# Kernel tuning notes

Measured on AMD Instinct MI355X. Metric: run time of the kernel, lower is better.

The kernel has to match this reference:

```python
import jax, jax.numpy as jnp
import numpy as np

B, L, F, H, HDE, E, V, MH, MW, TOUT = 64, 2, 512, 512, 512, 512, 94, 6, 40, 30
V2 = V + 2          # vocab + START/END + NULL slots
T = TOUT + 2        # decode steps
HW = MH * MW
START = V + 1
END = V + 1


def setup_inputs() -> dict:
    key = jax.random.key(0)
    ks = jax.random.split(key, 20)
    s = 0.05  # weight scale for numerical stability
    n = lambda k, shape: jax.random.normal(k, shape, jnp.float32) * s
    d = {}
    d['conv_f'] = jax.random.normal(ks[0], (B, F, MH, MW), jnp.float32)
    d['target'] = jax.random.randint(ks[1], (B, TOUT), 0, 95, dtype=jnp.int32)
    d['w_ih_en'] = n(ks[2], (L, 4 * H, F))
    d['w_hh_en'] = n(ks[3], (L, 4 * H, H))
    d['b_ih_en'] = n(ks[4], (L, 4 * H))
    d['b_hh_en'] = n(ks[5], (L, 4 * H))
    d['embed_w'] = n(ks[6], (V2, H))
    d['w_ih_de'] = n(ks[7], (L, 4 * HDE, H))
    d['w_hh_de'] = n(ks[8], (L, 4 * HDE, HDE))
    d['b_ih_de'] = n(ks[9], (L, 4 * HDE))
    d['b_hh_de'] = n(ks[10], (L, 4 * HDE))
    d['att_wh'] = n(ks[11], (E, HDE))
    d['att_bh'] = n(ks[12], (E,))
    d['att_conv_w'] = n(ks[13], (E, F, 3, 3))
    d['att_conv_b'] = n(ks[14], (E,))
    d['att_wv'] = n(ks[15], (1, E))
    d['att_bv'] = n(ks[16], (1,))
    d['out_w'] = n(ks[17], (V2, HDE + F))
    d['out_b'] = n(ks[18], (V2,))
    return d


def _lstm_cell(x, h, c, wih, whh, bih, bhh):
    # PyTorch gate order: i, f, g, o
    g = x @ wih.T + h @ whh.T + bih + bhh
    i, f, gg, o = jnp.split(g, 4, axis=-1)
    c_new = jax.nn.sigmoid(f) * c + jax.nn.sigmoid(i) * jnp.tanh(gg)
    h_new = jax.nn.sigmoid(o) * jnp.tanh(c_new)
    return h_new, c_new


def _forward(conv_f, target, w_ih_en, w_hh_en, b_ih_en, b_hh_en, embed_w,
             w_ih_de, w_hh_de, b_ih_de, b_hh_de, att_wh, att_bh,
             att_conv_w, att_conv_b, att_wv, att_bv, out_w, out_b):
    # ---- encoder: maxpool over full height, then 2-layer LSTM over width ----
    x_seq = jnp.max(conv_f, axis=2).transpose(2, 0, 1)  # [W, B, F]

    def enc_step(carry, xt):
        h, c = carry
        inp = xt
        hs, cs = [], []
        for l in range(L):
            hl, cl = _lstm_cell(inp, h[l], c[l], w_ih_en[l], w_hh_en[l],
                                b_ih_en[l], b_hh_en[l])
            inp = hl
            hs.append(hl); cs.append(cl)
        return (jnp.stack(hs), jnp.stack(cs)), inp

    z = jnp.zeros((L, B, H), conv_f.dtype)
    _, enc_out = jax.lax.scan(enc_step, (z, z), x_seq)
    holistic = enc_out[-1]  # [B, H]

    # ---- attention: conv_f embedding computed ONCE (invariant across steps) ----
    xe = jax.lax.conv_general_dilated(
        conv_f, att_conv_w, (1, 1), 'SAME',
        dimension_numbers=('NCHW', 'OIHW', 'NCHW')) + att_conv_b[None, :, None, None]
    x_em = xe.reshape(B, E, HW).transpose(0, 2, 1)       # [B, HW, E]
    cf_flat = conv_f.reshape(B, F, HW).transpose(0, 2, 1)  # [B, HW, F]

    # ---- decoder inputs: t=0 holistic, t>=1 embed(gt_with_start[:, t-1]) ----
    gt = jnp.concatenate(
        [jnp.full((B, 1), START, dtype=target.dtype), target], axis=1)  # [B, T-1]
    xs = jnp.concatenate([holistic[None], embed_w[gt.T]], axis=0)  # [T, B, H]

    def dec_step(carry, xt):
        h, c = carry
        inp = xt
        hs, cs = [], []
        for l in range(L):
            hl, cl = _lstm_cell(inp, h[l], c[l], w_ih_de[l], w_hh_de[l],
                                b_ih_de[l], b_hh_de[l])
            inp = hl
            hs.append(hl); cs.append(cl)
        hlast = inp  # [B, HDE]
        g_em = hlast @ att_wh.T + att_bh                    # [B, E]
        feat = jnp.tanh(x_em + g_em[:, None, :])            # [B, HW, E] (dropout=identity)
        e = feat @ att_wv[0] + att_bv[0]                    # [B, HW]
        alpha = jax.nn.softmax(e, axis=-1)
        att = jnp.einsum('bw,bwf->bf', alpha, cf_flat)      # [B, F]
        logits = jnp.concatenate([hlast, att], axis=-1) @ out_w.T + out_b
        scores = jax.nn.log_softmax(logits, axis=-1)        # [B, V2]
        return (jnp.stack(hs), jnp.stack(cs)), scores

    zd = jnp.zeros((B, HDE), conv_f.dtype)
    z0 = jnp.stack([zd] * L)
    _, out_tbv = jax.lax.scan(dec_step, (z0, z0), xs)  # [T, B, V2]
    out = out_tbv.transpose(1, 0, 2)                    # [B, T, V2]

    # ---- build l_target: [0, target..., 0] with first padding 0 -> END ----
    l_target = jnp.zeros((B, T), jnp.int32).at[:, 1:-1].set(target)
    j = jnp.argmax(l_target[:, 1:] == 0, axis=1) + 1  # first zero at col>=1 (always exists)
    l_target = l_target.at[jnp.arange(B), j].set(END)

    # ---- masked NLL loss ----
    lt = l_target.reshape(-1)
    nll = -out.reshape(-1, V2)[jnp.arange(B * T), lt]
    mask = (lt != 0).astype(out.dtype)
    return jnp.sum(nll * mask) / jnp.sum(mask)


def reference(conv_f, target, w_ih_en, w_hh_en, b_ih_en, b_hh_en, embed_w,
              w_ih_de, w_hh_de, b_ih_de, b_hh_de, att_wh, att_bh,
              att_conv_w, att_conv_b, att_wv, att_bv, out_w, out_b):
    return _forward(conv_f, target, w_ih_en, w_hh_en, b_ih_en, b_hh_en, embed_w,
                    w_ih_de, w_hh_de, b_ih_de, b_hh_de, att_wh, att_bh,
                    att_conv_w, att_conv_b, att_wv, att_bv, out_w, out_b)
```

## Files before the change

### kernel.cpp

```cpp
#include <hip/hip_runtime.h>

typedef __fp16 f16;
typedef __fp16 f16x4 __attribute__((ext_vector_type(4)));
typedef __fp16 f16x8 __attribute__((ext_vector_type(8)));
typedef float  f32x4 __attribute__((ext_vector_type(4)));
typedef unsigned long long ull;

#define DEV static __device__ __forceinline__

DEV f32x4 mfma16(f16x4 a, f16x4 b, f32x4 c) {
  return __builtin_amdgcn_mfma_f32_16x16x16f16(a, b, c, 0, 0, 0);
}
DEV f16x4 lo4(f16x8 v) { return __builtin_shufflevector(v, v, 0, 1, 2, 3); }
DEV f16x4 hi4(f16x8 v) { return __builtin_shufflevector(v, v, 4, 5, 6, 7); }
DEV float sigf(float x) { return 1.f / (1.f + __expf(-x)); }
DEV float tanh_(float x) { float e = __expf(2.f * x); return 1.f - 2.f / (e + 1.f); }

union U8 { float4 f4; float2 f2[2]; };
union H2 { unsigned u; f16 h[2]; };
union H4 { ull u; f16 h[4]; f16x4 v; };

#define HB 32768

DEV ull ldU(const ull* p) {
  return __hip_atomic_load(p, __ATOMIC_RELAXED, __HIP_MEMORY_SCOPE_AGENT);
}
DEV unsigned ldF(const unsigned* p) {
  return __hip_atomic_load(p, __ATOMIC_RELAXED, __HIP_MEMORY_SCOPE_AGENT);
}
DEV void stU32(unsigned* p, unsigned v) {
  __hip_atomic_store(p, v, __ATOMIC_RELAXED, __HIP_MEMORY_SCOPE_AGENT);
}
DEV void stU64(ull* p, ull v) {
  __hip_atomic_store(p, v, __ATOMIC_RELAXED, __HIP_MEMORY_SCOPE_AGENT);
}

DEV void wait8(const unsigned* line, unsigned tgt) {
  if (threadIdx.x < 8)
    while (ldF(line + threadIdx.x * 16) < tgt) {}
  __syncthreads();
}

DEV void signalDone(unsigned* line, int slot) {
  asm volatile("s_waitcnt vmcnt(0)" ::: "memory");
  __syncthreads();
  if (threadIdx.x == 0)
    __hip_atomic_fetch_add(line + slot * 16, 1u, __ATOMIC_RELAXED, __HIP_MEMORY_SCOPE_AGENT);
}

DEV void stageRow(const f16* __restrict__ s, f16* __restrict__ dstRow, int ch) {
  U8 u0, u1;
  u0.f4 = *(const float4*)s;
  u1.f4 = *(const float4*)(s + 8);
  *(float2*)(dstRow +  0 + ch * 4) = u0.f2[0];
  *(float2*)(dstRow + 16 + ch * 4) = u0.f2[1];
  *(float2*)(dstRow + 32 + ch * 4) = u1.f2[0];
  *(float2*)(dstRow + 48 + ch * 4) = u1.f2[1];
}

DEV void stageAu(const ull* __restrict__ srcU, f16 (*A)[64][72], int tid) {
  int row = tid >> 2, ch = tid & 3;
  const ull* s = srcU + row * 128 + ch * 4;
#pragma unroll
  for (int c = 0; c < 8; ++c) {
    ull d0 = ldU(s + c * 16 + 0);
    ull d1 = ldU(s + c * 16 + 1);
    ull d2 = ldU(s + c * 16 + 2);
    ull d3 = ldU(s + c * 16 + 3);
    f16* d = &A[c][row][0];
    *(ull*)(d +  0 + ch * 4) = d0;
    *(ull*)(d + 16 + ch * 4) = d1;
    *(ull*)(d + 32 + ch * 4) = d2;
    *(ull*)(d + 48 + ch * 4) = d3;
  }
}

DEV void kloop32(const f16 (*Wt)[32][72], const f16 (*A)[64][72],
                 int mh, int ns, int m16, int g4, f32x4 acc[2]) {
#pragma unroll
  for (int c = 0; c < 8; ++c) {
#pragma unroll
    for (int half = 0; half < 2; ++half) {
      f16x8 bf = *(const f16x8*)&Wt[c][ns * 16 + m16][g4 * 16 + half * 8];
      f16x4 bl = lo4(bf), bh = hi4(bf);
#pragma unroll
      for (int mt = 0; mt < 2; ++mt) {
        f16x8 af = *(const f16x8*)&A[c][mh * 32 + mt * 16 + m16][g4 * 16 + half * 8];
        acc[mt] = mfma16(lo4(af), bl, acc[mt]);
        acc[mt] = mfma16(hi4(af), bh, acc[mt]);
      }
    }
  }
}

DEV void kloop64(const f16* Wg, const f16 (*A)[64][72],
                 int nsG, int m16, int g4, f32x4 acc[4]) {
#pragma unroll
  for (int c = 0; c < 8; ++c) {
#pragma unroll
    for (int half = 0; half < 2; ++half) {
      f16x8 bf = *(const f16x8*)&Wg[((size_t)(c * 64 + nsG * 16 + m16)) * 72 + g4 * 16 + half * 8];
      f16x4 bl = lo4(bf), bh = hi4(bf);
#pragma unroll
      for (int mt = 0; mt < 4; ++mt) {
        f16x8 af = *(const f16x8*)&A[c][mt * 16 + m16][g4 * 16 + half * 8];
        acc[mt] = mfma16(lo4(af), bl, acc[mt]);
        acc[mt] = mfma16(hi4(af), bh, acc[mt]);
      }
    }
  }
}

DEV void convTile(char* smem, int tile, const f16* __restrict__ cfT,
                  const f16* __restrict__ wc9, const float* __restrict__ cb,
                  f16* __restrict__ xemH) {
  f16 (*At)[40] = (f16(*)[40])smem;
  f16 (*Bt)[40] = (f16(*)[40])(smem + 19200);
  const int t = threadIdx.x, lane = t & 63, w = t >> 6;
  const int b = tile >> 2, eb = (tile & 3) * 128;
  const int m16 = lane & 15, g4 = lane >> 4;
  f32x4 acc[15][2] = {};

  for (int kr = 0; kr < 9; ++kr) {
    int dh = kr / 3 - 1, dw = kr % 3 - 1;
    for (int f0 = 0; f0 < 512; f0 += 32) {
      __syncthreads();
      if (t < 240) {
        int hh = t / 40 + dh, ww = t % 40 + dw;
        if (hh >= 0 && hh < 6 && ww >= 0 && ww < 40) {
          const f16* s = cfT + ((size_t)(b * 240 + hh * 40 + ww) * 512 + f0);
          U8 u0, u1, u2, u3;
          u0.f4 = *(const float4*)s;        u1.f4 = *(const float4*)(s + 8);
          u2.f4 = *(const float4*)(s + 16); u3.f4 = *(const float4*)(s + 24);
          *(float2*)&At[t][ 0] = u0.f2[0];
          *(float2*)&At[t][ 8] = u0.f2[1];
          *(float2*)&At[t][16] = u1.f2[0];
          *(float2*)&At[t][24] = u1.f2[1];
          *(float2*)&At[t][ 4] = u2.f2[0];
          *(float2*)&At[t][12] = u2.f2[1];
          *(float2*)&At[t][20] = u3.f2[0];
          *(float2*)&At[t][28] = u3.f2[1];
        } else {
          float2 z = make_float2(0.f, 0.f);
          *(float2*)&At[t][ 0] = z; *(float2*)&At[t][ 8] = z;
          *(float2*)&At[t][16] = z; *(float2*)&At[t][24] = z;
          *(float2*)&At[t][ 4] = z; *(float2*)&At[t][12] = z;
          *(float2*)&At[t][20] = z; *(float2*)&At[t][28] = z;
        }
      }
      {
        int n = t >> 1, ch = t & 1;
        const f16* s = wc9 + (size_t)(eb + n) * 4608 + kr * 512 + f0 + ch * 16;
        U8 u0, u1;
        u0.f4 = *(const float4*)s; u1.f4 = *(const float4*)(s + 8);
        *(float2*)&Bt[n][ 0 + ch * 4] = u0.f2[0];
        *(float2*)&Bt[n][ 8 + ch * 4] = u0.f2[1];
        *(float2*)&Bt[n][16 + ch * 4] = u1.f2[0];
        *(float2*)&Bt[n][24 + ch * 4] = u1.f2[1];
      }
      __syncthreads();
      f16x8 b0 = *(const f16x8*)&Bt[w * 32 + m16][g4 * 8];
      f16x8 b1v = *(const f16x8*)&Bt[w * 32 + 16 + m16][g4 * 8];
      f16x4 b0l = lo4(b0), b0h = hi4(b0), b1l = lo4(b1v), b1h = hi4(b1v);
#pragma unroll
      for (int mt = 0; mt < 15; ++mt) {
        f16x8 af = *(const f16x8*)&At[mt * 16 + m16][g4 * 8];
        f16x4 al = lo4(af), ah = hi4(af);
        acc[mt][0] = mfma16(al, b0l, acc[mt][0]);
        acc[mt][1] = mfma16(al, b1l, acc[mt][1]);
        acc[mt][0] = mfma16(ah, b0h, acc[mt][0]);
        acc[mt][1] = mfma16(ah, b1h, acc[mt][1]);
      }
    }
  }
#pragma unroll
  for (int nt = 0; nt < 2; ++nt) {
    int e = eb + w * 32 + nt * 16 + m16;
    float bias = cb[e];
#pragma unroll
    for (int mt = 0; mt < 15; ++mt)
#pragma unroll
      for (int r = 0; r < 4; ++r) {
        int p = mt * 16 + g4 * 4 + r;
        xemH[((size_t)(b * 240 + p)) * 512 + e] = (f16)(acc[mt][nt][r] + bias);
      }
  }
}


__global__ void k_convert4(const float* __restrict__ src, f16* __restrict__ dst, int n4) {
  int i = blockIdx.x * 256 + threadIdx.x;
  if (i < n4) {
    float4 v = ((const float4*)src)[i];
    f16x4 o = { (f16)v.x, (f16)v.y, (f16)v.z, (f16)v.w };
    *(f16x4*)(dst + (size_t)i * 4) = o;
  }
}

__global__ void k_convW(const float* __restrict__ s0, const float* __restrict__ s1,
                        const float* __restrict__ s2, const float* __restrict__ s3,
                        f16* __restrict__ d0, f16* __restrict__ d1,
                        f16* __restrict__ d2, f16* __restrict__ d3) {
  int i = blockIdx.x * 256 + threadIdx.x;
  int sel = i >> 19, j = i & 524287;
  const float* s = sel == 0 ? s0 : sel == 1 ? s1 : sel == 2 ? s2 : s3;
  f16* d = sel == 0 ? d0 : sel == 1 ? d1 : sel == 2 ? d2 : d3;
  float4 v = ((const float4*)s)[j];
  f16x4 o = { (f16)v.x, (f16)v.y, (f16)v.z, (f16)v.w };
  *(f16x4*)(d + (size_t)j * 4) = o;
}

__global__ void k_wc9(const float* __restrict__ src, f16* __restrict__ dst) {
  int i = blockIdx.x * 256 + threadIdx.x;
  if (i < 512 * 4608) {
    int e = i / 4608, k = i % 4608;
    int rr = k / 512, f = k % 512;
    dst[i] = (f16)src[(size_t)e * 4608 + f * 9 + rr];
  }
}

__global__ __launch_bounds__(256) void k_cfmx(
    const float* __restrict__ cf, f16* __restrict__ cfT, f16* __restrict__ xseq)
{
  __shared__ float sT[64][244];
  const int tid = threadIdx.x;
  const int f0 = blockIdx.x * 64, b = blockIdx.y;
  const float* src = cf + ((size_t)b * 512 + f0) * 240;
  for (int i = tid; i < 3840; i += 256) {
    float4 v = ((const float4*)src)[i];
    int fl = i / 60, pc = (i % 60) * 4;
    sT[fl][pc] = v.x; sT[fl][pc + 1] = v.y; sT[fl][pc + 2] = v.z; sT[fl][pc + 3] = v.w;
  }
  __syncthreads();
  if (tid < 240) {
    int p = tid;
    f16* drow = cfT + ((size_t)b * 240 + p) * 512 + f0;
#pragma unroll
    for (int j = 0; j < 8; ++j) {
      f16x8 o;
#pragma unroll
      for (int k = 0; k < 8; ++k) o[k] = (f16)sT[j * 8 + k][p];
      *(f16x8*)(drow + j * 8) = o;
    }
  }
  {
    int fl = tid >> 2, wq = tid & 3;
#pragma unroll
    for (int wi = 0; wi < 10; ++wi) {
      int w = wq * 10 + wi;
      float m = sT[fl][w];
#pragma unroll
      for (int h = 1; h < 6; ++h) m = fmaxf(m, sT[fl][h * 40 + w]);
      xseq[((size_t)w * 64 + b) * 512 + f0 + fl] = (f16)m;
    }
  }
}

__global__ void k_ltarget(const int* __restrict__ target, int* __restrict__ lt) {
  int b = threadIdx.x;
  if (b >= 64) return;
  int row[32];
  row[0] = 0;
  for (int t = 1; t <= 30; ++t) row[t] = target[b * 30 + t - 1];
  row[31] = 0;
  int j = 1;
  while (row[j] != 0) ++j;
  row[j] = 95;
  for (int t = 0; t < 32; ++t) lt[b * 32 + t] = row[t];
}

__global__ void k_fill_xs(const f16* __restrict__ hol, const f16* __restrict__ emb,
                          const int* __restrict__ tgt, f16* __restrict__ xs) {
  int i = blockIdx.x * 256 + threadIdx.x;
  if (i < 32 * 64 * 512) {
    int t = i / (64 * 512), r = i % (64 * 512);
    int b = r / 512, u = r % 512;
    f16 v;
    if (t == 0) v = hol[b * 512 + u];
    else {
      int tok = (t == 1) ? 95 : tgt[b * 30 + t - 2];
      v = emb[(size_t)tok * 512 + u];
    }
    xs[i] = v;
  }
}

__global__ __launch_bounds__(256) void k_gemmX(
    const f16* __restrict__ A, const f16* __restrict__ W,
    const float* __restrict__ b1, const float* __restrict__ b2,
    f16* __restrict__ C)
{
  __shared__ f16 At[64][72];
  __shared__ f16 Bt[64][72];
  const int t = threadIdx.x, lane = t & 63, g = t >> 6;
  f32x4 acc[4] = {};
  const int m16 = lane & 15, g4 = lane >> 4;
  const size_t arow0 = (size_t)blockIdx.x * 64;

  for (int k0 = 0; k0 < 512; k0 += 64) {
    __syncthreads();
    { int row = t >> 2, ch = t & 3;
      stageRow(A + (arow0 + row) * 512 + k0 + ch * 16, &At[row][0], ch); }
    { int row = t >> 2, ch = t & 3;
      stageRow(W + ((size_t)blockIdx.y * 64 + row) * 512 + k0 + ch * 16, &Bt[row][0], ch); }
    __syncthreads();
#pragma unroll
    for (int half = 0; half < 2; ++half) {
      f16x8 bf = *(const f16x8*)&Bt[g * 16 + m16][g4 * 16 + half * 8];
      f16x4 bl = lo4(bf), bh = hi4(bf);
#pragma unroll
      for (int mt = 0; mt < 4; ++mt) {
        f16x8 af = *(const f16x8*)&At[mt * 16 + m16][g4 * 16 + half * 8];
        acc[mt] = mfma16(lo4(af), bl, acc[mt]);
        acc[mt] = mfma16(hi4(af), bh, acc[mt]);
      }
    }
  }
  int e = blockIdx.y * 64 + g * 16 + m16;
  float bias = b1[e] + b2[e];
#pragma unroll
  for (int mt = 0; mt < 4; ++mt)
#pragma unroll
    for (int r = 0; r < 4; ++r)
      C[(arow0 + mt * 16 + g4 * 4 + r) * 2048 + e] = (f16)(acc[mt][r] + bias);
}

__global__ __launch_bounds__(256) void k_gemmG(
    const f16* __restrict__ A, const f16* __restrict__ W,
    const float* __restrict__ b1, f16* __restrict__ C)
{
  __shared__ f16 At[64][72];
  __shared__ f16 Bt[64][72];
  const int t = threadIdx.x, lane = t & 63, g = t >> 6;
  f32x4 acc[4] = {};
  const int m16 = lane & 15, g4 = lane >> 4;
  const size_t arow0 = (size_t)blockIdx.x * 64;

  for (int k0 = 0; k0 < 512; k0 += 64) {
    __syncthreads();
    { int row = t >> 2, ch = t & 3;
      stageRow(A + (arow0 + row) * 512 + k0 + ch * 16, &At[row][0], ch); }
    { int row = t >> 2, ch = t & 3;
      stageRow(W + ((size_t)blockIdx.y * 64 + row) * 512 + k0 + ch * 16, &Bt[row][0], ch); }
    __syncthreads();
#pragma unroll
    for (int half = 0; half < 2; ++half) {
      f16x8 bf = *(const f16x8*)&Bt[g * 16 + m16][g4 * 16 + half * 8];
      f16x4 bl = lo4(bf), bh = hi4(bf);
#pragma unroll
      for (int mt = 0; mt < 4; ++mt) {
        f16x8 af = *(const f16x8*)&At[mt * 16 + m16][g4 * 16 + half * 8];
        acc[mt] = mfma16(lo4(af), bl, acc[mt]);
        acc[mt] = mfma16(hi4(af), bh, acc[mt]);
      }
    }
  }
  int e = blockIdx.y * 64 + g * 16 + m16;
  float bias = b1[e];
#pragma unroll
  for (int mt = 0; mt < 4; ++mt)
#pragma unroll
    for (int r = 0; r < 4; ++r)
      C[(arow0 + mt * 16 + g4 * 4 + r) * 512 + e] = (f16)(acc[mt][r] + bias);
}

__global__ __launch_bounds__(256) void k_gemmL(
    const f16* __restrict__ A, const f16* __restrict__ W,
    const float* __restrict__ bias, float* __restrict__ C)
{
  __shared__ f16 At[64][72];
  __shared__ f16 Bt[64][72];
  const int t = threadIdx.x, lane = t & 63, g = t >> 6;
  f32x4 acc[4] = {};
  const int m16 = lane & 15, g4 = lane >> 4;
  const size_t arow0 = (size_t)blockIdx.x * 64;

  for (int k0 = 0; k0 < 1024; k0 += 64) {
    __syncthreads();
    { int row = t >> 2, ch = t & 3;
      stageRow(A + (arow0 + row) * 1024 + k0 + ch * 16, &At[row][0], ch); }
    { int row = t >> 2, ch = t & 3;
      stageRow(W + ((size_t)(blockIdx.y * 64 + row)) * 1024 + k0 + ch * 16, &Bt[row][0], ch); }
    __syncthreads();
#pragma unroll
    for (int half = 0; half < 2; ++half) {
      f16x8 bf = *(const f16x8*)&Bt[g * 16 + m16][g4 * 16 + half * 8];
      f16x4 bl = lo4(bf), bh = hi4(bf);
#pragma unroll
      for (int mt = 0; mt < 4; ++mt) {
        f16x8 af = *(const f16x8*)&At[mt * 16 + m16][g4 * 16 + half * 8];
        acc[mt] = mfma16(lo4(af), bl, acc[mt]);
        acc[mt] = mfma16(hi4(af), bh, acc[mt]);
      }
    }
  }
  int e = blockIdx.y * 64 + g * 16 + m16;
  if (e < 96) {
    float be = bias[e];
#pragma unroll
    for (int mt = 0; mt < 4; ++mt)
#pragma unroll
      for (int r = 0; r < 4; ++r)
        C[(arow0 + mt * 16 + g4 * 4 + r) * 96 + e] = acc[mt][r] + be;
  }
}

__global__ __launch_bounds__(256, 1) void k_lstm(
    int T,
    const f16* __restrict__ G0, const f16* __restrict__ whh0,
    const f16* __restrict__ wih1, const f16* __restrict__ whh1,
    const float* __restrict__ bih1, const float* __restrict__ bhh1,
    f16* __restrict__ h0seq, f16* __restrict__ h1seq,
    unsigned* __restrict__ cnt,
    const f16* __restrict__ cfT, const f16* __restrict__ wc9,
    const float* __restrict__ cb, f16* __restrict__ xemH, int convBase)
{
  __shared__ __align__(16) char smem[147456];
  const int tid = threadIdx.x, lane = tid & 63, w = tid >> 6;
  const int m16 = lane & 15, g4 = lane >> 4;
  const int bid = blockIdx.x;

  if (bid >= 96) {
    convTile(smem, convBase + bid - 96, cfT, wc9, cb, xemH);
    return;
  }

  if (bid < 32) {
    f16 (*sW)[64][72] = (f16(*)[64][72])smem;
    f16 (*sA)[64][72] = (f16(*)[64][72])(smem + 73728);
    float* sG = (float*)(smem + 73728);
    const int utile = bid;
    { int r = tid >> 2, ch = tid & 3;
      int grow = (r >> 4) * 512 + utile * 16 + (r & 15);
      for (int c = 0; c < 8; ++c)
        stageRow(whh0 + (size_t)grow * 512 + c * 64 + ch * 16, &sW[c][r][0], ch);
    }
    const int pb = tid >> 2, uq = tid & 3;
    float cst[4] = {0.f, 0.f, 0.f, 0.f};
    for (int t = 0; t < T; ++t) {
      if (t > 0) wait8(cnt + (t - 1) * 128, 4);
      stageAu((const ull*)h0seq + (size_t)t * 8192, sA, tid);
      __syncthreads();
      f32x4 acc[4] = {};
      kloop64((const f16*)sW, sA, w, m16, g4, acc);
      __syncthreads();
#pragma unroll
      for (int mt = 0; mt < 4; ++mt)
#pragma unroll
        for (int r = 0; r < 4; ++r)
          sG[((size_t)w * 64 + mt * 16 + g4 * 4 + r) * 17 + m16] = acc[mt][r];
      __syncthreads();
      {
        const f16* gp = G0 + ((size_t)(t * 64 + pb)) * 2048 + utile * 16 + uq * 4;
        H4 gI, gF, gG, gO, outp;
        gI.v = *(const f16x4*)(gp);
        gF.v = *(const f16x4*)(gp + 512);
        gG.v = *(const f16x4*)(gp + 1024);
        gO.v = *(const f16x4*)(gp + 1536);
#pragma unroll
        for (int j = 0; j < 4; ++j) {
          int u = uq * 4 + j;
          float gi = sG[(0 * 64 + pb) * 17 + u] + (float)gI.h[j];
          float gf = sG[(1 * 64 + pb) * 17 + u] + (float)gF.h[j];
          float gg = sG[(2 * 64 + pb) * 17 + u] + (float)gG.h[j];
          float go = sG[(3 * 64 + pb) * 17 + u] + (float)gO.h[j];
          float cn = sigf(gf) * cst[j] + sigf(gi) * tanh_(gg);
          float hn = sigf(go) * tanh_(cn);
          cst[j] = cn;
          outp.h[j] = (f16)hn;
        }
        stU64((ull*)h0seq + (size_t)(t + 1) * 8192 + pb * 128 + utile * 4 + uq, outp.u);
      }
      signalDone(cnt + t * 128, bid & 7);
    }
  } else {
    f16 (*sW2)[8][32][72] = (f16(*)[8][32][72])smem;
    f16 (*sA)[64][72] = (f16(*)[64][72])(smem + 73728);
    float* sG = (float*)(smem + 73728);
    const int utile = bid - 32;
    const int mh = w >> 1, ns = w & 1;
    { int mat = tid >> 7;
      int r = (tid >> 2) & 31, ch = tid & 3;
      int grow = (r >> 3) * 512 + utile * 8 + (r & 7);
      const f16* Wsrc = (mat == 0) ? wih1 : whh1;
      for (int c = 0; c < 8; ++c)
        stageRow(Wsrc + (size_t)grow * 512 + c * 64 + ch * 16, &sW2[mat][c][r][0], ch);
    }
    const int pb = tid >> 2, pup = tid & 3;
    float badd[4][2];
#pragma unroll
    for (int g = 0; g < 4; ++g)
#pragma unroll
      for (int j = 0; j < 2; ++j) {
        int rr = g * 512 + utile * 8 + pup * 2 + j;
        badd[g][j] = bih1[rr] + bhh1[rr];
      }
    float cst[2] = {0.f, 0.f};
    unsigned* line1 = cnt + (size_t)T * 128;
    for (int t = 0; t < T; ++t) {
      wait8(cnt + t * 128, 4);
      stageAu((const ull*)h0seq + (size_t)(t + 1) * 8192, sA, tid);
      if (t > 0) wait8(line1 + (t - 1) * 128, 8);
      else       __syncthreads();
      ull rg[8][4];
      { const ull* s1p = (const ull*)h1seq + (size_t)t * 8192 + (tid >> 2) * 128 + (tid & 3) * 4;
#pragma unroll
        for (int c = 0; c < 8; ++c)
#pragma unroll
          for (int q = 0; q < 4; ++q) rg[c][q] = ldU(s1p + c * 16 + q);
      }
      f32x4 acc[2] = {};
      kloop32(sW2[0], sA, mh, ns, m16, g4, acc);
      __syncthreads();
      { int row = tid >> 2, ch = tid & 3;
#pragma unroll
        for (int c = 0; c < 8; ++c) {
          f16* d = &sA[c][row][0];
          *(ull*)(d +  0 + ch * 4) = rg[c][0];
          *(ull*)(d + 16 + ch * 4) = rg[c][1];
          *(ull*)(d + 32 + ch * 4) = rg[c][2];
          *(ull*)(d + 48 + ch * 4) = rg[c][3];
        }
      }
      __syncthreads();
      kloop32(sW2[1], sA, mh, ns, m16, g4, acc);
      __syncthreads();
      { int nl = ns * 16 + m16;
#pragma unroll
        for (int mt = 0; mt < 2; ++mt)
#pragma unroll
          for (int r = 0; r < 4; ++r) {
            int b = mh * 32 + mt * 16 + g4 * 4 + r;
            sG[((nl >> 3) * 64 + b) * 9 + (nl & 7)] = acc[mt][r];
          }
      }
      __syncthreads();
      {
        H2 outp;
#pragma unroll
        for (int j = 0; j < 2; ++j) {
          int u = pup * 2 + j;
          float gi = sG[(0 * 64 + pb) * 9 + u] + badd[0][j];
          float gf = sG[(1 * 64 + pb) * 9 + u] + badd[1][j];
          float gg = sG[(2 * 64 + pb) * 9 + u] + badd[2][j];
          float go = sG[(3 * 64 + pb) * 9 + u] + badd[3][j];
          float cn = sigf(gf) * cst[j] + sigf(gi) * tanh_(gg);
          float hn = sigf(go) * tanh_(cn);
          cst[j] = cn;
          outp.h[j] = (f16)hn;
        }
        stU32((unsigned*)h1seq + (size_t)(t + 1) * 16384 + pb * 256 + utile * 4 + pup, outp.u);
      }
      signalDone(line1 + t * 128, bid & 7);
    }
  }
}


__global__ __launch_bounds__(256) void k_scoreAll(
    const f16* __restrict__ xemH, const f16* __restrict__ gAll,
    const float* __restrict__ wv, float* __restrict__ esc)
{
  __shared__ f16 sX[20][512];
  const int tid = threadIdx.x, lane = tid & 63, w = tid >> 6;
  const int tile = blockIdx.x, b = blockIdx.y;
  for (int i = tid; i < 20 * 64; i += 256) {
    int row = i >> 6, seg = i & 63;
    *(f16x8*)&sX[row][seg * 8] =
        *(const f16x8*)(xemH + ((size_t)(b * 240 + tile * 20 + row)) * 512 + seg * 8);
  }
  float w8[8];
  { const float4* wp = (const float4*)(wv + lane * 8);
    float4 wa = wp[0], wb = wp[1];
    w8[0] = wa.x; w8[1] = wa.y; w8[2] = wa.z; w8[3] = wa.w;
    w8[4] = wb.x; w8[5] = wb.y; w8[6] = wb.z; w8[7] = wb.w; }
  __syncthreads();
  for (int t = 0; t < 32; ++t) {
    f16x8 gv = *(const f16x8*)(gAll + ((size_t)(t * 64 + b)) * 512 + lane * 8);
    float g8[8];
#pragma unroll
    for (int j = 0; j < 8; ++j) g8[j] = (float)gv[j];
#pragma unroll
    for (int i = 0; i < 5; ++i) {
      int rr = i * 4 + w;
      f16x8 xv = *(const f16x8*)&sX[rr][lane * 8];
      float s = 0.f;
#pragma unroll
      for (int j = 0; j < 8; ++j) s += tanh_((float)xv[j] + g8[j]) * w8[j];
#pragma unroll
      for (int m = 32; m; m >>= 1) s += __shfl_xor(s, m);
      if (lane == 0) esc[((size_t)(t * 64 + b)) * 240 + tile * 20 + rr] = s;
    }
  }
}

__global__ __launch_bounds__(256) void k_smctx(
    const float* __restrict__ esc, const f16* __restrict__ cfT,
    const f16* __restrict__ h1seq, f16* __restrict__ ctx)
{
  __shared__ float aAl[8][240];
  const int tid = threadIdx.x, lane = tid & 63, w = tid >> 6;
  const int tq = blockIdx.x, b = blockIdx.y;
  for (int half = 0; half < 2; ++half) {
    int tt = w + half * 4;
    int t = tq * 8 + tt;
    const float* er = esc + ((size_t)(t * 64 + b)) * 240;
    float v[4];
    float mx = -1e30f;
#pragma unroll
    for (int q = 0; q < 4; ++q) {
      int p = lane + q * 64;
      v[q] = (p < 240) ? er[p] : -1e30f;
      mx = fmaxf(mx, v[q]);
    }
#pragma unroll
    for (int m = 32; m; m >>= 1) mx = fmaxf(mx, __shfl_xor(mx, m));
    float sum = 0.f;
#pragma unroll
    for (int q = 0; q < 4; ++q) { v[q] = __expf(v[q] - mx); sum += v[q]; }
#pragma unroll
    for (int m = 32; m; m >>= 1) sum += __shfl_xor(sum, m);
    float inv = 1.f / sum;
#pragma unroll
    for (int q = 0; q < 4; ++q) {
      int p = lane + q * 64;
      if (p < 240) aAl[tt][p] = v[q] * inv;
    }
  }
  __syncthreads();
  float acc[8][2] = {};
  const f16* cb = cfT + (size_t)b * 240 * 512;
  for (int p = 0; p < 240; ++p) {
    H2 cw; cw.u = *(const unsigned*)(cb + (size_t)p * 512 + tid * 2);
    float c0 = (float)cw.h[0], c1 = (float)cw.h[1];
#pragma unroll
    for (int tt = 0; tt < 8; ++tt) {
      float a = aAl[tt][p];
      acc[tt][0] += a * c0;
      acc[tt][1] += a * c1;
    }
  }
#pragma unroll
  for (int tt = 0; tt < 8; ++tt) {
    int t = tq * 8 + tt;
    size_t r = (size_t)(t * 64 + b);
    H2 o; o.h[0] = (f16)acc[tt][0]; o.h[1] = (f16)acc[tt][1];
    *(unsigned*)(ctx + r * 1024 + 512 + tid * 2) = o.u;
    *(unsigned*)(ctx + r * 1024 + tid * 2) =
        *(const unsigned*)(h1seq + (size_t)(t + 1) * HB + b * 512 + tid * 2);
  }
}

__global__ void k_nllloss(const float* __restrict__ lgt, const int* __restrict__ ltg,
                          float* __restrict__ out) {
  __shared__ float sa[256], sb[256];
  int tid = threadIdx.x;
  float a = 0.f, m = 0.f;
  for (int r = tid; r < 2048; r += 256) {
    int t = r >> 6, b = r & 63;
    int tok = ltg[b * 32 + t];
    if (tok != 0) {
      const float* row = lgt + (size_t)r * 96;
      float mx = -1e30f;
      for (int j = 0; j < 96; ++j) mx = fmaxf(mx, row[j]);
      float s = 0.f;
      for (int j = 0; j < 96; ++j) s += __expf(row[j] - mx);
      a += mx + __logf(s) - row[tok];
      m += 1.f;
    }
  }
  sa[tid] = a; sb[tid] = m; __syncthreads();
  for (int s = 128; s; s >>= 1) { if (tid < s) { sa[tid] += sa[tid + s]; sb[tid] += sb[tid + s]; } __syncthreads(); }
  if (tid == 0) out[0] = sa[0] / sb[0];
}


extern "C" void kernel_launch(void* const* d_in, const int* in_sizes, int n_in,
                              void* d_out, int out_size, void* d_ws, size_t ws_size,
                              hipStream_t stream) {
  (void)in_sizes; (void)n_in; (void)out_size; (void)ws_size;
  const float* conv_f = (const float*)d_in[0];
  const int*   target = (const int*)d_in[1];
  const float* wih_en = (const float*)d_in[2];
  const float* whh_en = (const float*)d_in[3];
  const float* bih_en = (const float*)d_in[4];
  const float* bhh_en = (const float*)d_in[5];
  const float* embed  = (const float*)d_in[6];
  const float* wih_de = (const float*)d_in[7];
  const float* whh_de = (const float*)d_in[8];
  const float* bih_de = (const float*)d_in[9];
  const float* bhh_de = (const float*)d_in[10];
  const float* att_wh = (const float*)d_in[11];
  const float* att_bh = (const float*)d_in[12];
  const float* att_cw = (const float*)d_in[13];
  const float* att_cb = (const float*)d_in[14];
  const float* att_wv = (const float*)d_in[15];
  const float* out_w  = (const float*)d_in[17];
  const float* out_b  = (const float*)d_in[18];
  float* out = (float*)d_out;

  size_t o = 0;
  char* base = (char*)d_ws;
  auto take = [&](size_t bytes) -> void* {
    void* p = base + o;
    o += (bytes + 255) & ~(size_t)255;
    return p;
  };
  const size_t WSZ = (size_t)2048 * 512;
  f16* wihEn = (f16*)take(2 * WSZ * 2);
  f16* whhEn = (f16*)take(2 * WSZ * 2);
  f16* wihDe = (f16*)take(2 * WSZ * 2);
  f16* whhDe = (f16*)take(2 * WSZ * 2);
  f16* awh   = (f16*)take((size_t)512 * 512 * 2);
  f16* emb   = (f16*)take((size_t)96 * 512 * 2);
  f16* wc9   = (f16*)take((size_t)512 * 4608 * 2);
  f16* cfT   = (f16*)take((size_t)64 * 240 * 512 * 2);
  f16* xseq  = (f16*)take((size_t)40 * 64 * 512 * 2);
  f16* xs    = (f16*)take((size_t)32 * 64 * 512 * 2);
  f16* xemH  = (f16*)take((size_t)64 * 240 * 512 * 2);
  f16* outwH = (f16*)take((size_t)128 * 1024 * 2);
  f16* X0en  = (f16*)take((size_t)2560 * 2048 * 2);
  f16* X0de  = (f16*)take((size_t)2048 * 2048 * 2);
  f16* h0seqE = (f16*)take((size_t)41 * HB * 2);
  f16* h1seqE = (f16*)take((size_t)41 * HB * 2);
  f16* h0seqD = (f16*)take((size_t)33 * HB * 2);
  f16* h1seqD = (f16*)take((size_t)33 * HB * 2);
  f16* gAll   = (f16*)take((size_t)2048 * 512 * 2);
  int*   ltg   = (int*)take((size_t)2048 * 4);
  unsigned* cntE = (unsigned*)take(65536);
  unsigned* cntD = (unsigned*)take(65536);
  float* escAll = (float*)X0en;
  float* lgtAll = (float*)((char*)X0en + 4194304);
  f16*   ctxAll = X0de;

  k_convW<<<8192, 256, 0, stream>>>(wih_en, whh_en, wih_de, whh_de,
                                    wihEn, whhEn, wihDe, whhDe);
  k_convert4<<<256, 256, 0, stream>>>(att_wh, awh, 512 * 512 / 4);
  k_convert4<<<48, 256, 0, stream>>>(embed, emb, 96 * 512 / 4);
  k_convert4<<<96, 256, 0, stream>>>(out_w, outwH, 96 * 1024 / 4);
  k_wc9<<<(512 * 4608 + 255) / 256, 256, 0, stream>>>(att_cw, wc9);
  k_cfmx<<<dim3(8, 64), 256, 0, stream>>>(conv_f, cfT, xseq);
  k_ltarget<<<1, 64, 0, stream>>>(target, ltg);
  hipMemsetAsync(h0seqE, 0, (size_t)HB * 2, stream);
  hipMemsetAsync(h1seqE, 0, (size_t)HB * 2, stream);
  hipMemsetAsync(h0seqD, 0, (size_t)HB * 2, stream);
  hipMemsetAsync(h1seqD, 0, (size_t)HB * 2, stream);
  hipMemsetAsync(cntE, 0, 131072, stream);

  k_gemmX<<<dim3(40, 32), 256, 0, stream>>>(xseq, wihEn, bih_en, bhh_en, X0en);

  k_lstm<<<224, 256, 0, stream>>>(40, X0en, whhEn, wihEn + WSZ, whhEn + WSZ,
                                  bih_en + 2048, bhh_en + 2048, h0seqE, h1seqE, cntE,
                                  cfT, wc9, att_cb, xemH, 0);

  k_fill_xs<<<(32 * 64 * 512 + 255) / 256, 256, 0, stream>>>(h1seqE + (size_t)40 * HB, emb, target, xs);
  k_gemmX<<<dim3(32, 32), 256, 0, stream>>>(xs, wihDe, bih_de, bhh_de, X0de);

  k_lstm<<<224, 256, 0, stream>>>(32, X0de, whhDe, wihDe + WSZ, whhDe + WSZ,
                                  bih_de + 2048, bhh_de + 2048, h0seqD, h1seqD, cntD,
                                  cfT, wc9, att_cb, xemH, 128);

  k_gemmG<<<dim3(32, 8), 256, 0, stream>>>(h1seqD + HB, awh, att_bh, gAll);
  k_scoreAll<<<dim3(12, 64), 256, 0, stream>>>(xemH, gAll, att_wv, escAll);
  k_smctx<<<dim3(4, 64), 256, 0, stream>>>(escAll, cfT, h1seqD, ctxAll);
  k_gemmL<<<dim3(32, 2), 256, 0, stream>>>(ctxAll, outwH, out_b, lgtAll);
  k_nllloss<<<1, 256, 0, stream>>>(lgtAll, ltg, out);
}
```

Baseline: 906.5 us.

## Fuse input-projection and attention GEMMs into persistent LSTM kernel with wave-level signaling

Moves the layer-0 input projection GEMM (X·Wih) and the attention-query GEMM into dedicated producer/consumer blocks inside the persistent LSTM kernel, synchronised through global counters, so they overlap with the recurrence instead of running as separate launches. Signalling becomes per-wave instead of per-block, which removes a block barrier before each flag increment; wait thresholds are scaled to match. It also merges small conversion, zeroing and l_target kernels, and stages the conv-weight transpose through shared memory. The risk is extra spin-wait latency on the serial critical path and more blocks competing for CUs.

Measured after the change: 1.045 ms. +15.2%, slower.

```diff
diff --git a/kernel.cpp b/kernel.cpp
--- a/kernel.cpp
+++ b/kernel.cpp
@@ -41,10 +41,9 @@
   __syncthreads();
 }
 
-DEV void signalDone(unsigned* line, int slot) {
+DEV void signalWave(unsigned* line, int slot) {
   asm volatile("s_waitcnt vmcnt(0)" ::: "memory");
-  __syncthreads();
-  if (threadIdx.x == 0)
+  if ((threadIdx.x & 63) == 0)
     __hip_atomic_fetch_add(line + slot * 16, 1u, __ATOMIC_RELAXED, __HIP_MEMORY_SCOPE_AGENT);
 }
 
@@ -56,6 +55,14 @@
   *(float2*)(dstRow + 16 + ch * 4) = u0.f2[1];
   *(float2*)(dstRow + 32 + ch * 4) = u1.f2[0];
   *(float2*)(dstRow + 48 + ch * 4) = u1.f2[1];
+}
+
+DEV void stageAc(const f16* __restrict__ src, f16 (*A)[64][72], int tid) {
+  int row = tid >> 2, ch = tid & 3;
+  const f16* s = src + (size_t)row * 512 + ch * 16;
+#pragma unroll
+  for (int c = 0; c < 8; ++c)
+    stageRow(s + c * 64, &A[c][row][0], ch);
 }
 
 DEV void stageAu(const ull* __restrict__ srcU, f16 (*A)[64][72], int tid) {
@@ -188,15 +195,6 @@
 }
 
 
-__global__ void k_convert4(const float* __restrict__ src, f16* __restrict__ dst, int n4) {
-  int i = blockIdx.x * 256 + threadIdx.x;
-  if (i < n4) {
-    float4 v = ((const float4*)src)[i];
-    f16x4 o = { (f16)v.x, (f16)v.y, (f16)v.z, (f16)v.w };
-    *(f16x4*)(dst + (size_t)i * 4) = o;
-  }
-}
-
 __global__ void k_convW(const float* __restrict__ s0, const float* __restrict__ s1,
                         const float* __restrict__ s2, const float* __restrict__ s3,
                         f16* __restrict__ d0, f16* __restrict__ d1,
@@ -210,12 +208,29 @@
   *(f16x4*)(d + (size_t)j * 4) = o;
 }
 
-__global__ void k_wc9(const float* __restrict__ src, f16* __restrict__ dst) {
+__global__ void k_convS(const float* __restrict__ awhS, const float* __restrict__ embS,
+                        const float* __restrict__ outwS,
+                        f16* __restrict__ awhD, f16* __restrict__ embD,
+                        f16* __restrict__ outwD) {
   int i = blockIdx.x * 256 + threadIdx.x;
-  if (i < 512 * 4608) {
-    int e = i / 4608, k = i % 4608;
-    int rr = k / 512, f = k % 512;
-    dst[i] = (f16)src[(size_t)e * 4608 + f * 9 + rr];
+  const float* s; f16* d; int j;
+  if (i < 65536) { s = awhS; d = awhD; j = i; }
+  else if (i < 65536 + 12288) { s = embS; d = embD; j = i - 65536; }
+  else if (i < 65536 + 12288 + 24576) { s = outwS; d = outwD; j = i - 65536 - 12288; }
+  else return;
+  float4 v = ((const float4*)s)[j];
+  f16x4 o = { (f16)v.x, (f16)v.y, (f16)v.z, (f16)v.w };
+  *(f16x4*)(d + (size_t)j * 4) = o;
+}
+
+__global__ __launch_bounds__(256) void k_wc9(const float* __restrict__ src, f16* __restrict__ dst) {
+  __shared__ float s[4608];
+  const int e = blockIdx.x, tid = threadIdx.x;
+  for (int i = tid; i < 4608; i += 256) s[i] = src[(size_t)e * 4608 + i];
+  __syncthreads();
+  for (int j = tid; j < 4608; j += 256) {
+    int rr = j >> 9, f = j & 511;
+    dst[(size_t)e * 4608 + j] = (f16)s[f * 9 + rr];
   }
 }
 
@@ -256,162 +271,37 @@
   }
 }
 
-__global__ void k_ltarget(const int* __restrict__ target, int* __restrict__ lt) {
-  int b = threadIdx.x;
-  if (b >= 64) return;
-  int row[32];
-  row[0] = 0;
-  for (int t = 1; t <= 30; ++t) row[t] = target[b * 30 + t - 1];
-  row[31] = 0;
-  int j = 1;
-  while (row[j] != 0) ++j;
-  row[j] = 95;
-  for (int t = 0; t < 32; ++t) lt[b * 32 + t] = row[t];
-}
-
-__global__ void k_fill_xs(const f16* __restrict__ hol, const f16* __restrict__ emb,
-                          const int* __restrict__ tgt, f16* __restrict__ xs) {
+__global__ void k_zero(unsigned* p0, unsigned* p1, unsigned* p2,
+                       unsigned* p3, unsigned* p4, unsigned* p5) {
   int i = blockIdx.x * 256 + threadIdx.x;
-  if (i < 32 * 64 * 512) {
-    int t = i / (64 * 512), r = i % (64 * 512);
-    int b = r / 512, u = r % 512;
-    f16 v;
-    if (t == 0) v = hol[b * 512 + u];
-    else {
-      int tok = (t == 1) ? 95 : tgt[b * 30 + t - 2];
-      v = emb[(size_t)tok * 512 + u];
-    }
-    xs[i] = v;
-  }
-}
-
-__global__ __launch_bounds__(256) void k_gemmX(
-    const f16* __restrict__ A, const f16* __restrict__ W,
-    const float* __restrict__ b1, const float* __restrict__ b2,
-    f16* __restrict__ C)
-{
-  __shared__ f16 At[64][72];
-  __shared__ f16 Bt[64][72];
-  const int t = threadIdx.x, lane = t & 63, g = t >> 6;
-  f32x4 acc[4] = {};
-  const int m16 = lane & 15, g4 = lane >> 4;
-  const size_t arow0 = (size_t)blockIdx.x * 64;
-
-  for (int k0 = 0; k0 < 512; k0 += 64) {
-    __syncthreads();
-    { int row = t >> 2, ch = t & 3;
-      stageRow(A + (arow0 + row) * 512 + k0 + ch * 16, &At[row][0], ch); }
-    { int row = t >> 2, ch = t & 3;
-      stageRow(W + ((size_t)blockIdx.y * 64 + row) * 512 + k0 + ch * 16, &Bt[row][0], ch); }
-    __syncthreads();
-#pragma unroll
-    for (int half = 0; half < 2; ++half) {
-      f16x8 bf = *(const f16x8*)&Bt[g * 16 + m16][g4 * 16 + half * 8];
-      f16x4 bl = lo4(bf), bh = hi4(bf);
-#pragma unroll
-      for (int mt = 0; mt < 4; ++mt) {
-        f16x8 af = *(const f16x8*)&At[mt * 16 + m16][g4 * 16 + half * 8];
-        acc[mt] = mfma16(lo4(af), bl, acc[mt]);
-        acc[mt] = mfma16(hi4(af), bh, acc[mt]);
-      }
-    }
-  }
-  int e = blockIdx.y * 64 + g * 16 + m16;
-  float bias = b1[e] + b2[e];
-#pragma unroll
-  for (int mt = 0; mt < 4; ++mt)
-#pragma unroll
-    for (int r = 0; r < 4; ++r)
-      C[(arow0 + mt * 16 + g4 * 4 + r) * 2048 + e] = (f16)(acc[mt][r] + bias);
-}
-
-__global__ __launch_bounds__(256) void k_gemmG(
-    const f16* __restrict__ A, const f16* __restrict__ W,
-    const float* __restrict__ b1, f16* __restrict__ C)
-{
-  __shared__ f16 At[64][72];
-  __shared__ f16 Bt[64][72];
-  const int t = threadIdx.x, lane = t & 63, g = t >> 6;
-  f32x4 acc[4] = {};
-  const int m16 = lane & 15, g4 = lane >> 4;
-  const size_t arow0 = (size_t)blockIdx.x * 64;
-
-  for (int k0 = 0; k0 < 512; k0 += 64) {
-    __syncthreads();
-    { int row = t >> 2, ch = t & 3;
-      stageRow(A + (arow0 + row) * 512 + k0 + ch * 16, &At[row][0], ch); }
-    { int row = t >> 2, ch = t & 3;
-      stageRow(W + ((size_t)blockIdx.y * 64 + row) * 512 + k0 + ch * 16, &Bt[row][0], ch); }
-    __syncthreads();
-#pragma unroll
-    for (int half = 0; half < 2; ++half) {
-      f16x8 bf = *(const f16x8*)&Bt[g * 16 + m16][g4 * 16 + half * 8];
-      f16x4 bl = lo4(bf), bh = hi4(bf);
-#pragma unroll
-      for (int mt = 0; mt < 4; ++mt) {
-        f16x8 af = *(const f16x8*)&At[mt * 16 + m16][g4 * 16 + half * 8];
-        acc[mt] = mfma16(lo4(af), bl, acc[mt]);
-        acc[mt] = mfma16(hi4(af), bh, acc[mt]);
-      }
-    }
-  }
-  int e = blockIdx.y * 64 + g * 16 + m16;
-  float bias = b1[e];
-#pragma unroll
-  for (int mt = 0; mt < 4; ++mt)
-#pragma unroll
-    for (int r = 0; r < 4; ++r)
-      C[(arow0 + mt * 16 + g4 * 4 + r) * 512 + e] = (f16)(acc[mt][r] + bias);
-}
-
-__global__ __launch_bounds__(256) void k_gemmL(
-    const f16* __restrict__ A, const f16* __restrict__ W,
-    const float* __restrict__ bias, float* __restrict__ C)
-{
-  __shared__ f16 At[64][72];
-  __shared__ f16 Bt[64][72];
-  const int t = threadIdx.x, lane = t & 63, g = t >> 6;
-  f32x4 acc[4] = {};
-  const int m16 = lane & 15, g4 = lane >> 4;
-  const size_t arow0 = (size_t)blockIdx.x * 64;
-
-  for (int k0 = 0; k0 < 1024; k0 += 64) {
-    __syncthreads();
-    { int row = t >> 2, ch = t & 3;
-      stageRow(A + (arow0 + row) * 1024 + k0 + ch * 16, &At[row][0], ch); }
-    { int row = t >> 2, ch = t & 3;
-      stageRow(W + ((size_t)(blockIdx.y * 64 + row)) * 1024 + k0 + ch * 16, &Bt[row][0], ch); }
-    __syncthreads();
-#pragma unroll
-    for (int half = 0; half < 2; ++half) {
-      f16x8 bf = *(const f16x8*)&Bt[g * 16 + m16][g4 * 16 + half * 8];
-      f16x4 bl = lo4(bf), bh = hi4(bf);
-#pragma unroll
-      for (int mt = 0; mt < 4; ++mt) {
-        f16x8 af = *(const f16x8*)&At[mt * 16 + m16][g4 * 16 + half * 8];
-        acc[mt] = mfma16(lo4(af), bl, acc[mt]);
-        acc[mt] = mfma16(hi4(af), bh, acc[mt]);
-      }
-    }
-  }
-  int e = blockIdx.y * 64 + g * 16 + m16;
-  if (e < 96) {
-    float be = bias[e];
-#pragma unroll
-    for (int mt = 0; mt < 4; ++mt)
-#pragma unroll
-      for (int r = 0; r < 4; ++r)
-        C[(arow0 + mt * 16 + g4 * 4 + r) * 96 + e] = acc[mt][r] + be;
+  int sel = i >> 14, j = i & 16383;
+  unsigned* p = sel == 0 ? p0 : sel == 1 ? p1 : sel == 2 ? p2 :
+                sel == 3 ? p3 : sel == 4 ? p4 : p5;
+  p[j] = 0;
+}
+
+__global__ void k_fill_xs_emb(const f16* __restrict__ emb, const int* __restrict__ tgt,
+                              f16* __restrict__ xs) {
+  int i = blockIdx.x * 256 + threadIdx.x;
+  if (i < 31 * HB) {
+    int t = 1 + i / HB, r = i % HB;
+    int b = r >> 9, u = r & 511;
+    int tok = (t == 1) ? 95 : tgt[b * 30 + t - 2];
+    xs[(size_t)t * HB + r] = emb[(size_t)tok * 512 + u];
   }
 }
 
 __global__ __launch_bounds__(256, 1) void k_lstm(
-    int T,
-    const f16* __restrict__ G0, const f16* __restrict__ whh0,
+    int T, int mode,
+    const f16* __restrict__ xbase, const f16* __restrict__ x_t0,
+    const f16* __restrict__ wih0, const float* __restrict__ bih0, const float* __restrict__ bhh0,
+    f16* __restrict__ G0,
+    const f16* __restrict__ whh0,
     const f16* __restrict__ wih1, const f16* __restrict__ whh1,
     const float* __restrict__ bih1, const float* __restrict__ bhh1,
     f16* __restrict__ h0seq, f16* __restrict__ h1seq,
     unsigned* __restrict__ cnt,
+    const f16* __restrict__ awh, const float* __restrict__ gbias, f16* __restrict__ gAll,
     const f16* __restrict__ cfT, const f16* __restrict__ wc9,
     const float* __restrict__ cb, f16* __restrict__ xemH, int convBase)
 {
@@ -420,25 +310,29 @@
   const int m16 = lane & 15, g4 = lane >> 4;
   const int bid = blockIdx.x;
 
-  if (bid >= 96) {
-    convTile(smem, convBase + bid - 96, cfT, wc9, cb, xemH);
-    return;
-  }
-
   if (bid < 32) {
     f16 (*sW)[64][72] = (f16(*)[64][72])smem;
     f16 (*sA)[64][72] = (f16(*)[64][72])(smem + 73728);
     float* sG = (float*)(smem + 73728);
-    const int utile = bid;
+    const int utile = bid, pb = tid >> 2, uq = tid & 3;
     { int r = tid >> 2, ch = tid & 3;
       int grow = (r >> 4) * 512 + utile * 16 + (r & 15);
       for (int c = 0; c < 8; ++c)
         stageRow(whh0 + (size_t)grow * 512 + c * 64 + ch * 16, &sW[c][r][0], ch);
     }
-    const int pb = tid >> 2, uq = tid & 3;
     float cst[4] = {0.f, 0.f, 0.f, 0.f};
     for (int t = 0; t < T; ++t) {
-      if (t > 0) wait8(cnt + (t - 1) * 128, 4);
+      {
+        const unsigned* lineA = cnt + (size_t)(t > 0 ? t - 1 : 0) * 128;
+        const unsigned* lineX = cnt + (size_t)(2 * T + t) * 128;
+        unsigned tA = (t > 0) ? 16u : 0u;
+        if (tid < 8) { while (tA && ldF(lineA + tid * 16) < tA) {} }
+        else if (tid < 16) { while (ldF(lineX + (tid - 8) * 16) < 4u) {} }
+        __syncthreads();
+      }
+      const ull* gp = (const ull*)G0 + (size_t)(t * 64 + pb) * 512 + utile * 4 + uq;
+      H4 gI, gF, gG, gO;
+      gI.u = ldU(gp); gF.u = ldU(gp + 128); gG.u = ldU(gp + 256); gO.u = ldU(gp + 384);
       stageAu((const ull*)h0seq + (size_t)t * 8192, sA, tid);
       __syncthreads();
       f32x4 acc[4] = {};
@@ -451,12 +345,7 @@
           sG[((size_t)w * 64 + mt * 16 + g4 * 4 + r) * 17 + m16] = acc[mt][r];
       __syncthreads();
       {
-        const f16* gp = G0 + ((size_t)(t * 64 + pb)) * 2048 + utile * 16 + uq * 4;
-        H4 gI, gF, gG, gO, outp;
-        gI.v = *(const f16x4*)(gp);
-        gF.v = *(const f16x4*)(gp + 512);
-        gG.v = *(const f16x4*)(gp + 1024);
-        gO.v = *(const f16x4*)(gp + 1536);
+        H4 outp;
 #pragma unroll
         for (int j = 0; j < 4; ++j) {
           int u = uq * 4 + j;
@@ -471,9 +360,9 @@
         }
         stU64((ull*)h0seq + (size_t)(t + 1) * 8192 + pb * 128 + utile * 4 + uq, outp.u);
       }
-      signalDone(cnt + t * 128, bid & 7);
-    }
-  } else {
+      signalWave(cnt + (size_t)t * 128, bid & 7);
+    }
+  } else if (bid < 96) {
     f16 (*sW2)[8][32][72] = (f16(*)[8][32][72])smem;
     f16 (*sA)[64][72] = (f16(*)[64][72])(smem + 73728);
     float* sG = (float*)(smem + 73728);
@@ -498,9 +387,9 @@
     float cst[2] = {0.f, 0.f};
     unsigned* line1 = cnt + (size_t)T * 128;
     for (int t = 0; t < T; ++t) {
-      wait8(cnt + t * 128, 4);
+      wait8(cnt + (size_t)t * 128, 16);
       stageAu((const ull*)h0seq + (size_t)(t + 1) * 8192, sA, tid);
-      if (t > 0) wait8(line1 + (t - 1) * 128, 8);
+      if (t > 0) wait8(line1 + (size_t)(t - 1) * 128, 32);
       else       __syncthreads();
       ull rg[8][4];
       { const ull* s1p = (const ull*)h1seq + (size_t)t * 8192 + (tid >> 2) * 128 + (tid & 3) * 4;
@@ -551,7 +440,80 @@
         }
         stU32((unsigned*)h1seq + (size_t)(t + 1) * 16384 + pb * 256 + utile * 4 + pup, outp.u);
       }
-      signalDone(line1 + t * 128, bid & 7);
+      signalWave(line1 + (size_t)t * 128, bid & 7);
+    }
+  } else if (bid < 128) {
+    const int rid = bid - 96;
+    f16 (*sW)[64][72] = (f16(*)[64][72])smem;
+    f16 (*sA)[64][72] = (f16(*)[64][72])(smem + 73728);
+    { int r = tid >> 2, ch = tid & 3;
+      for (int c = 0; c < 8; ++c)
+        stageRow(wih0 + (size_t)(rid * 64 + r) * 512 + c * 64 + ch * 16, &sW[c][r][0], ch);
+    }
+    const int e = rid * 64 + w * 16 + m16;
+    const float bias_e = bih0[e] + bhh0[e];
+    __syncthreads();
+    for (int t = 0; t < T; ++t) {
+      const f16* Asrc = (t == 0) ? x_t0 : xbase + (size_t)t * HB;
+      stageAc(Asrc, sA, tid);
+      __syncthreads();
+      f32x4 acc[4] = {};
+      kloop64((const f16*)sW, sA, w, m16, g4, acc);
+      __syncthreads();
+      f16 (*sC)[72] = (f16(*)[72])sA;
+#pragma unroll
+      for (int mt = 0; mt < 4; ++mt)
+#pragma unroll
+        for (int r = 0; r < 4; ++r)
+          sC[mt * 16 + g4 * 4 + r][w * 16 + m16] = (f16)(acc[mt][r] + bias_e);
+      __syncthreads();
+#pragma unroll
+      for (int k = 0; k < 4; ++k) {
+        int id = tid * 4 + k;
+        int row = id >> 4, c4 = id & 15;
+        H4 pk; pk.v = *(const f16x4*)&sC[row][c4 * 4];
+        stU64((ull*)G0 + (size_t)(t * 64 + row) * 512 + rid * 16 + c4, pk.u);
+      }
+      asm volatile("s_waitcnt vmcnt(0)" ::: "memory");
+      __syncthreads();
+      if (tid == 0)
+        __hip_atomic_fetch_add(cnt + (size_t)(2 * T + t) * 128 + (rid & 7) * 16, 1u,
+                               __ATOMIC_RELAXED, __HIP_MEMORY_SCOPE_AGENT);
+      __syncthreads();
+    }
+  } else if (mode == 1 && bid < 136) {
+    const int g = bid - 128;
+    f16* sWg = (f16*)smem;
+    f16 (*sA)[64][72] = (f16(*)[64][72])(smem + 73728);
+    { int r = tid >> 2, ch = tid & 3;
+      for (int c = 0; c < 8; ++c)
+        stageRow(awh + (size_t)(g * 64 + r) * 512 + c * 64 + ch * 16,
+                 sWg + ((size_t)(c * 64 + r)) * 72, ch);
+    }
+    const int e = g * 64 + w * 16 + m16;
+    const float gb = gbias[e];
+    __syncthreads();
+    unsigned* line1 = cnt + (size_t)T * 128;
+    for (int t = 0; t < T; ++t) {
+      wait8(line1 + (size_t)t * 128, 32);
+      stageAu((const ull*)h1seq + (size_t)(t + 1) * 8192, sA, tid);
+      __syncthreads();
+      f32x4 acc[4] = {};
+      kloop64(sWg, sA, w, m16, g4, acc);
+      __syncthreads();
+#pragma unroll
+      for (int mt = 0; mt < 4; ++mt)
+#pragma unroll
+        for (int r = 0; r < 4; ++r)
+          gAll[(size_t)(t * 64 + mt * 16 + g4 * 4 + r) * 512 + e] = (f16)(acc[mt][r] + gb);
+    }
+  } else {
+    if (mode == 0) {
+      convTile(smem, convBase + bid - 128, cfT, wc9, cb, xemH);
+    } else {
+      int j = bid - 136;
+      convTile(smem, 128 + j, cfT, wc9, cb, xemH);
+      if (j < 8) { __syncthreads(); convTile(smem, 248 + j, cfT, wc9, cb, xemH); }
     }
   }
 }
@@ -651,10 +613,64 @@
   }
 }
 
-__global__ void k_nllloss(const float* __restrict__ lgt, const int* __restrict__ ltg,
+__global__ __launch_bounds__(256) void k_gemmL(
+    const f16* __restrict__ A, const f16* __restrict__ W,
+    const float* __restrict__ bias, float* __restrict__ C)
+{
+  __shared__ f16 At[64][72];
+  __shared__ f16 Bt[64][72];
+  const int t = threadIdx.x, lane = t & 63, g = t >> 6;
+  f32x4 acc[4] = {};
+  const int m16 = lane & 15, g4 = lane >> 4;
+  const size_t arow0 = (size_t)blockIdx.x * 64;
+
+  for (int k0 = 0; k0 < 1024; k0 += 64) {
+    __syncthreads();
+    { int row = t >> 2, ch = t & 3;
+      stageRow(A + (arow0 + row) * 1024 + k0 + ch * 16, &At[row][0], ch); }
+    { int row = t >> 2, ch = t & 3;
+      stageRow(W + ((size_t)(blockIdx.y * 64 + row)) * 1024 + k0 + ch * 16, &Bt[row][0], ch); }
+    __syncthreads();
+#pragma unroll
+    for (int half = 0; half < 2; ++half) {
+      f16x8 bf = *(const f16x8*)&Bt[g * 16 + m16][g4 * 16 + half * 8];
+      f16x4 bl = lo4(bf), bh = hi4(bf);
+#pragma unroll
+      for (int mt = 0; mt < 4; ++mt) {
+        f16x8 af = *(const f16x8*)&At[mt * 16 + m16][g4 * 16 + half * 8];
+        acc[mt] = mfma16(lo4(af), bl, acc[mt]);
+        acc[mt] = mfma16(hi4(af), bh, acc[mt]);
+      }
+    }
+  }
+  int e = blockIdx.y * 64 + g * 16 + m16;
+  if (e < 96) {
+    float be = bias[e];
+#pragma unroll
+    for (int mt = 0; mt < 4; ++mt)
+#pragma unroll
+      for (int r = 0; r < 4; ++r)
+        C[(arow0 + mt * 16 + g4 * 4 + r) * 96 + e] = acc[mt][r] + be;
+  }
+}
+
+__global__ void k_nllloss(const float* __restrict__ lgt, const int* __restrict__ target,
                           float* __restrict__ out) {
+  __shared__ int ltg[2048];
   __shared__ float sa[256], sb[256];
   int tid = threadIdx.x;
+  if (tid < 64) {
+    int b = tid;
+    int row[32];
+    row[0] = 0;
+    for (int t = 1; t <= 30; ++t) row[t] = target[b * 30 + t - 1];
+    row[31] = 0;
+    int j = 1;
+    while (row[j] != 0) ++j;
+    row[j] = 95;
+    for (int t = 0; t < 32; ++t) ltg[b * 32 + t] = row[t];
+  }
+  __syncthreads();
   float a = 0.f, m = 0.f;
   for (int r = tid; r < 2048; r += 256) {
     int t = r >> 6, b = r & 63;
@@ -726,7 +742,6 @@
   f16* h0seqD = (f16*)take((size_t)33 * HB * 2);
   f16* h1seqD = (f16*)take((size_t)33 * HB * 2);
   f16* gAll   = (f16*)take((size_t)2048 * 512 * 2);
-  int*   ltg   = (int*)take((size_t)2048 * 4);
   unsigned* cntE = (unsigned*)take(65536);
   unsigned* cntD = (unsigned*)take(65536);
   float* escAll = (float*)X0en;
@@ -735,34 +750,31 @@
 
   k_convW<<<8192, 256, 0, stream>>>(wih_en, whh_en, wih_de, whh_de,
                                     wihEn, whhEn, wihDe, whhDe);
-  k_convert4<<<256, 256, 0, stream>>>(att_wh, awh, 512 * 512 / 4);
-  k_convert4<<<48, 256, 0, stream>>>(embed, emb, 96 * 512 / 4);
-  k_convert4<<<96, 256, 0, stream>>>(out_w, outwH, 96 * 1024 / 4);
-  k_wc9<<<(512 * 4608 + 255) / 256, 256, 0, stream>>>(att_cw, wc9);
+  k_convS<<<400, 256, 0, stream>>>(att_wh, embed, out_w, awh, emb, outwH);
+  k_wc9<<<512, 256, 0, stream>>>(att_cw, wc9);
   k_cfmx<<<dim3(8, 64), 256, 0, stream>>>(conv_f, cfT, xseq);
-  k_ltarget<<<1, 64, 0, stream>>>(target, ltg);
-  hipMemsetAsync(h0seqE, 0, (size_t)HB * 2, stream);
-  hipMemsetAsync(h1seqE, 0, (size_t)HB * 2, stream);
-  hipMemsetAsync(h0seqD, 0, (size_t)HB * 2, stream);
-  hipMemsetAsync(h1seqD, 0, (size_t)HB * 2, stream);
-  hipMemsetAsync(cntE, 0, 131072, stream);
-
-  k_gemmX<<<dim3(40, 32), 256, 0, stream>>>(xseq, wihEn, bih_en, bhh_en, X0en);
-
-  k_lstm<<<224, 256, 0, stream>>>(40, X0en, whhEn, wihEn + WSZ, whhEn + WSZ,
-                                  bih_en + 2048, bhh_en + 2048, h0seqE, h1seqE, cntE,
+  k_zero<<<384, 256, 0, stream>>>((unsigned*)h0seqE, (unsigned*)h1seqE,
+                                  (unsigned*)h0seqD, (unsigned*)h1seqD, cntE, cntD);
+  k_fill_xs_emb<<<(31 * HB + 255) / 256, 256, 0, stream>>>(emb, target, xs);
+
+  k_lstm<<<256, 256, 0, stream>>>(40, 0, xseq, xseq,
+                                  wihEn, bih_en, bhh_en, X0en,
+                                  whhEn, wihEn + WSZ, whhEn + WSZ,
+                                  bih_en + 2048, bhh_en + 2048,
+                                  h0seqE, h1seqE, cntE,
+                                  nullptr, nullptr, nullptr,
                                   cfT, wc9, att_cb, xemH, 0);
 
-  k_fill_xs<<<(32 * 64 * 512 + 255) / 256, 256, 0, stream>>>(h1seqE + (size_t)40 * HB, emb, target, xs);
-  k_gemmX<<<dim3(32, 32), 256, 0, stream>>>(xs, wihDe, bih_de, bhh_de, X0de);
-
-  k_lstm<<<224, 256, 0, stream>>>(32, X0de, whhDe, wihDe + WSZ, whhDe + WSZ,
-                                  bih_de + 2048, bhh_de + 2048, h0seqD, h1seqD, cntD,
+  k_lstm<<<256, 256, 0, stream>>>(32, 1, xs, h1seqE + (size_t)40 * HB,
+                                  wihDe, bih_de, bhh_de, X0de,
+                                  whhDe, wihDe + WSZ, whhDe + WSZ,
+                                  bih_de + 2048, bhh_de + 2048,
+                                  h0seqD, h1seqD, cntD,
+                                  awh, att_bh, gAll,
                                   cfT, wc9, att_cb, xemH, 128);
 
-  k_gemmG<<<dim3(32, 8), 256, 0, stream>>>(h1seqD + HB, awh, att_bh, gAll);
   k_scoreAll<<<dim3(12, 64), 256, 0, stream>>>(xemH, gAll, att_wv, escAll);
   k_smctx<<<dim3(4, 64), 256, 0, stream>>>(escAll, cfT, h1seqD, ctxAll);
   k_gemmL<<<dim3(32, 2), 256, 0, stream>>>(ctxAll, outwH, out_b, lgtAll);
-  k_nllloss<<<1, 256, 0, stream>>>(lgtAll, ltg, out);
-}
+  k_nllloss<<<1, 256, 0, stream>>>(lgtAll, target, out);
+}
```
